# Kernel tuning notes

Measured on AMD Instinct MI355X. Metric: run time of the kernel, lower is better.

## Reference

```python
import jax, jax.numpy as jnp
import numpy as np

B, HH, WW = 8, 56, 56
N = HH * WW            # 3136 tokens
DIM, NH, SR = 512, 8, 7
HDIM = DIM // 2        # 256
LDIM = DIM - HDIM      # 256
DH = LDIM // NH        # 32
SCALE = DIM ** -0.5
EPS = 1e-5


def _dwconv(x, w):
    # depthwise 3x3, stride 1, SAME (= padding k//2): x [B,C,H,W], w [C,1,3,3]
    return jax.lax.conv_general_dilated(x, w, (1, 1), 'SAME',
                                        feature_group_count=x.shape[1],
                                        dimension_numbers=('NCHW', 'OIHW', 'NCHW'))


def _bn(x, g, b, m, v):
    # inference BatchNorm2d
    s = g * jax.lax.rsqrt(v + EPS)
    return (x - m[None, :, None, None]) * s[None, :, None, None] + b[None, :, None, None]


def _avg_pool(x, k):
    return jax.lax.reduce_window(x, 0.0, jax.lax.add, (1, 1, k, k), (1, 1, k, k), 'VALID') / (k * k)


def _max_pool(x, k):
    return jax.lax.reduce_window(x, -jnp.inf, jax.lax.max, (1, 1, k, k), (1, 1, k, k), 'VALID')


def setup_inputs() -> dict:
    key = jax.random.key(0)
    ks = jax.random.split(key, 32)
    d = {}
    d['x'] = jax.random.normal(ks[0], (B, N, DIM), jnp.float32)
    d['proj_v_w'] = jax.random.normal(ks[1], (LDIM, HDIM), jnp.float32) / np.sqrt(HDIM).astype(np.float32)
    d['conv1_w'] = jax.random.normal(ks[2], (LDIM, 1, 3, 3), jnp.float32) / 3.0
    d['conv2_w'] = jax.random.normal(ks[3], (LDIM, 1, 3, 3), jnp.float32) / 3.0
    d['conv3_w'] = jax.random.normal(ks[4], (HDIM, LDIM, 1, 1), jnp.float32) / np.sqrt(LDIM).astype(np.float32)
    d['conv3_b'] = jax.random.normal(ks[5], (HDIM,), jnp.float32) * 0.1
    d['v_conv_w'] = jax.random.normal(ks[6], (LDIM, 1, 3, 3), jnp.float32) / 3.0
    d['proj_w'] = jax.random.normal(ks[7], (DIM, DIM), jnp.float32) / np.sqrt(DIM).astype(np.float32)
    d['proj_b'] = jax.random.normal(ks[8], (DIM,), jnp.float32) * 0.1
    i = 9
    for pre, c in (('bn1', LDIM), ('bn2', LDIM), ('bn3', HDIM), ('vbn', LDIM)):
        d[pre + '_g'] = jax.random.uniform(ks[i], (c,), jnp.float32, 0.8, 1.2)
        d[pre + '_b'] = jax.random.normal(ks[i + 1], (c,), jnp.float32) * 0.1
        d[pre + '_m'] = jax.random.normal(ks[i + 2], (c,), jnp.float32) * 0.1
        d[pre + '_v'] = jax.random.uniform(ks[i + 3], (c,), jnp.float32, 0.5, 1.5)
        i += 4
    return d


def reference(x, proj_v_w, conv1_w, conv2_w, conv3_w, conv3_b, v_conv_w, proj_w, proj_b,
              bn1_g, bn1_b, bn1_m, bn1_v, bn2_g, bn2_b, bn2_m, bn2_v,
              bn3_g, bn3_b, bn3_m, bn3_v, vbn_g, vbn_b, vbn_m, vbn_v):
    x_high_in = x[..., :HDIM]                       # [B,N,HDIM]
    v = x_high_in @ proj_v_w.T                      # [B,N,LDIM]
    xh = v.reshape(B, HH, WW, LDIM).transpose(0, 3, 1, 2)   # [B,LDIM,H,W]
    xh = _bn(_dwconv(xh, conv1_w), bn1_g, bn1_b, bn1_m, bn1_v)
    q1 = _avg_pool(xh, SR)                          # [B,LDIM,8,8]
    q2 = _max_pool(xh, SR)
    xh = jax.nn.gelu(xh, approximate=False)
    xh = _bn(_dwconv(xh, conv2_w), bn2_g, bn2_b, bn2_m, bn2_v)
    k1 = _avg_pool(xh, SR)
    k2 = _max_pool(xh, SR)
    xh = jax.lax.conv_general_dilated(xh, conv3_w, (1, 1), 'SAME',
                                      dimension_numbers=('NCHW', 'OIHW', 'NCHW')) + conv3_b[None, :, None, None]
    xh = _bn(xh, bn3_g, bn3_b, bn3_m, bn3_v)
    xh = jax.nn.gelu(xh, approximate=False)
    x_high = xh.reshape(B, HDIM, N).transpose(0, 2, 1)      # [B,N,HDIM]

    hq, wq = HH // SR, WW // SR
    nq = hq * wq                                    # 64 pooled tokens

    def heads(t):                                   # [B,LDIM,hq,wq] -> [B,NH,nq,DH]
        return t.reshape(B, NH, DH, nq).transpose(0, 1, 3, 2)

    q = jnp.concatenate([heads(q1), heads(q2)], axis=-1)    # [B,NH,nq,2*DH]
    k = jnp.concatenate([heads(k1), heads(k2)], axis=-1)
    vh = v.reshape(B, N, NH, DH).transpose(0, 2, 1, 3)      # [B,NH,N,DH]

    attn = jnp.einsum('bhqd,bhkd->bhqk', q, k)              # [B,NH,nq,nq]
    attn = attn.reshape(B * NH, nq, hq, wq)
    attn = jax.image.resize(attn, (B * NH, nq, HH, WW), method='bilinear', antialias=False) * SCALE
    attn = attn.reshape(B, NH, nq, N)
    attn = jax.nn.softmax(attn, axis=-1)

    out = jnp.einsum('bhqn,bhnd->bhqd', attn, vh)           # [B,NH,nq,DH]
    out = out.reshape(B, NH, hq, wq, DH).transpose(0, 1, 4, 2, 3).reshape(B, LDIM, hq, wq)
    out = jax.image.resize(out, (B, LDIM, HH, WW), method='bilinear', antialias=False)
    out = _bn(_dwconv(out, v_conv_w), vbn_g, vbn_b, vbn_m, vbn_v)
    x_low = out.reshape(B, LDIM, N).transpose(0, 2, 1)      # [B,N,LDIM]

    y = jnp.concatenate([x_high, x_low], axis=-1) @ proj_w.T + proj_b
    return y
```

## Files before the change

### kernel.cpp

```cpp
#include <hip/hip_runtime.h>
#include <math.h>

#define BB 8
#define HH 56
#define WWD 56
#define NN 3136
#define CC 256
#define DIMM 512
#define NHEAD 8
#define NQ 64
#define EPSF 1e-5f
#define SCALEF 0.04419417382415922f

typedef __attribute__((ext_vector_type(8))) short short8;
typedef __attribute__((ext_vector_type(4))) short short4v;
typedef __attribute__((ext_vector_type(4))) float floatx4;

__device__ __forceinline__ float gelu_f(float x) {
    float z = x * 0.70710678118654752f;
    float a = fabsf(z);
    float t = __builtin_amdgcn_rcpf(1.f + 0.3275911f * a);
    float p = t * (0.254829592f + t * (-0.284496736f + t * (1.421413741f +
              t * (-1.453152027f + t * 1.061405429f))));
    float e = exp2f(-1.44269504f * a * a);
    float erfa = 1.f - p * e;
    float erfz = copysignf(erfa, z);
    return 0.5f * x * (1.f + erfz);
}
__device__ __forceinline__ unsigned short f2bf(float f) {
    union { float f; unsigned u; } v; v.f = f;
    return (unsigned short)((v.u + 0x7fffu + ((v.u >> 16) & 1u)) >> 16);
}
__device__ __forceinline__ float bf2f(unsigned short u) {
    union { unsigned u; float f; } v; v.u = ((unsigned)u) << 16;
    return v.f;
}

__global__ __launch_bounds__(256) void cast3_k(
    const float* __restrict__ a, const float* __restrict__ b,
    const float* __restrict__ cc, unsigned short* __restrict__ da,
    unsigned short* __restrict__ db, unsigned short* __restrict__ dc) {
    int i = blockIdx.x * 256 + threadIdx.x;
    if (i < 65536) {
        da[i] = f2bf(a[i]);
        db[i] = f2bf(b[i]);
    }
    if (i < 262144) dc[i] = f2bf(cc[i]);
}

__global__ __launch_bounds__(256) void gemm_v_mfma(
    const float* __restrict__ x, const unsigned short* __restrict__ w16,
    unsigned short* __restrict__ v16) {
    __shared__ short Ws[128 * 72];
    __shared__ short Xs[128 * 72];
    int n0 = blockIdx.x * 128, c0 = blockIdx.y * 128;
    int tid = threadIdx.x;
    int lane = tid & 63, wv = tid >> 6;
    int wc = wv >> 1, wn = wv & 1;
    int quad = lane >> 4, l16 = lane & 15;
    floatx4 zero = {0.f, 0.f, 0.f, 0.f};
    floatx4 acc[4][4];
#pragma unroll
    for (int ci = 0; ci < 4; ci++)
#pragma unroll
        for (int ni = 0; ni < 4; ni++) acc[ci][ni] = zero;

    for (int k0 = 0; k0 < 256; k0 += 64) {
        {
            int m = tid >> 1;
            int ob = (tid & 1) * 4;
            const float* src = x + (size_t)(n0 + m) * DIMM + k0 + ob * 8;
            short* dst = &Xs[m * 72 + ob * 8];
#pragma unroll
            for (int i2 = 0; i2 < 4; i2++) {
                floatx4 f0 = *(const floatx4*)(src + i2 * 8);
                floatx4 f1 = *(const floatx4*)(src + i2 * 8 + 4);
                short8 pk;
                pk[0] = (short)f2bf(f0[0]); pk[1] = (short)f2bf(f0[1]);
                pk[2] = (short)f2bf(f0[2]); pk[3] = (short)f2bf(f0[3]);
                pk[4] = (short)f2bf(f1[0]); pk[5] = (short)f2bf(f1[1]);
                pk[6] = (short)f2bf(f1[2]); pk[7] = (short)f2bf(f1[3]);
                *(short8*)(dst + i2 * 8) = pk;
            }
        }
#pragma unroll
        for (int i2 = 0; i2 < 4; i2++) {
            int idx = tid + 256 * i2;
            int c = idx >> 3, o = idx & 7;
            *(short8*)&Ws[c * 72 + o * 8] =
                *(const short8*)(const short*)(w16 + (size_t)(c0 + c) * 256 + k0 + o * 8);
        }
        __syncthreads();
#pragma unroll
        for (int kc = 0; kc < 2; kc++) {
            short8 af[4], bf[4];
#pragma unroll
            for (int ci = 0; ci < 4; ci++)
                af[ci] = *(const short8*)&Ws[(wc * 64 + ci * 16 + l16) * 72 + (kc * 4 + quad) * 8];
#pragma unroll
            for (int ni = 0; ni < 4; ni++)
                bf[ni] = *(const short8*)&Xs[(wn * 64 + ni * 16 + l16) * 72 + (kc * 4 + quad) * 8];
#pragma unroll
            for (int ci = 0; ci < 4; ci++)
#pragma unroll
                for (int ni = 0; ni < 4; ni++)
                    acc[ci][ni] = __builtin_amdgcn_mfma_f32_16x16x32_bf16(
                        af[ci], bf[ni], acc[ci][ni], 0, 0, 0);
        }
        __syncthreads();
    }
#pragma unroll
    for (int ni = 0; ni < 4; ni++) {
        int ng = n0 + wn * 64 + ni * 16 + l16;
        int b = ng / NN, n = ng - b * NN;
#pragma unroll
        for (int ci = 0; ci < 4; ci++) {
#pragma unroll
            for (int r = 0; r < 4; r++) {
                int c = c0 + wc * 64 + ci * 16 + quad * 4 + r;
                v16[((size_t)b * CC + c) * NN + n] = f2bf(acc[ci][ni][r]);
            }
        }
    }
}

__device__ __forceinline__ float dw3x3g(const float* __restrict__ Us, int lr,
                                        int x, bool ym, bool yp,
                                        float w0, float w1, float w2, float w3,
                                        float w4, float w5, float w6, float w7,
                                        float w8) {
    bool xm = x > 0, xp = x < 55;
    const float* r1 = &Us[(lr - 1) * 57 + x];
    const float* r2 = &Us[lr * 57 + x];
    const float* r3 = &Us[(lr + 1) * 57 + x];
    float acc = r2[0] * w4;
    if (xm) acc += r2[-1] * w3;
    if (xp) acc += r2[1] * w5;
    if (ym) {
        acc += r1[0] * w1;
        if (xm) acc += r1[-1] * w0;
        if (xp) acc += r1[1] * w2;
    }
    if (yp) {
        acc += r3[0] * w7;
        if (xm) acc += r3[-1] * w6;
        if (xp) acc += r3[1] * w8;
    }
    return acc;
}

__global__ __launch_bounds__(256) void dwconv2x_k(
    const unsigned short* __restrict__ in,
    const float* __restrict__ w1c, const float* __restrict__ g1,
    const float* __restrict__ b1, const float* __restrict__ m1,
    const float* __restrict__ v1,
    const float* __restrict__ w2c, const float* __restrict__ g2,
    const float* __restrict__ b2, const float* __restrict__ m2,
    const float* __restrict__ v2,
    unsigned short* __restrict__ out,
    float* __restrict__ oavg1, float* __restrict__ omax1,
    float* __restrict__ oavg2, float* __restrict__ omax2) {
    __shared__ float Us[18 * 57];
    __shared__ float Cs[16 * 57];
    int bid = blockIdx.x;
    int bc = bid >> 2, chunk = bid & 3;
    int c = bc & 255;
    int r0 = chunk * 14;
    int tid = threadIdx.x;
    const unsigned short* ip = in + (size_t)bc * NN;

    int gl0 = max(r0 - 2, 0), gh0 = min(r0 + 15, 55);
    int nin = (gh0 - gl0 + 1) * 56;
    const unsigned short* ipb = ip + gl0 * 56;
    {
        int e = tid * 4;
        if (e < nin) {
            short4v pk = *(const short4v*)(const short*)(ipb + e);
#pragma unroll
            for (int j = 0; j < 4; j++) {
                int el = e + j;
                int ry = el / 56, x = el - ry * 56;
                int lr = (gl0 + ry) - (r0 - 2);
                Us[lr * 57 + x] = bf2f((unsigned short)pk[j]);
            }
        }
    }
    float w0 = w1c[c * 9 + 0], w1 = w1c[c * 9 + 1], w2 = w1c[c * 9 + 2];
    float w3 = w1c[c * 9 + 3], w4 = w1c[c * 9 + 4], w5 = w1c[c * 9 + 5];
    float w6 = w1c[c * 9 + 6], w7 = w1c[c * 9 + 7], w8 = w1c[c * 9 + 8];
    float s = g1[c] * rsqrtf(v1[c] + EPSF);
    float sh = b1[c] - m1[c] * s;
    __syncthreads();
    int c1lo = max(r0 - 1, 0), c1hi = min(r0 + 14, 55);
    int n1 = (c1hi - c1lo + 1) * 56;
    for (int i = tid; i < n1; i += 256) {
        int ry = i / 56, x = i - ry * 56;
        int gr = c1lo + ry;
        int liu = gr - (r0 - 2);
        float acc = dw3x3g(Us, liu, x, gr > 0, gr < 55,
                           w0, w1, w2, w3, w4, w5, w6, w7, w8);
        Cs[(gr - (r0 - 1)) * 57 + x] = acc * s + sh;
    }
    __syncthreads();
    if (tid < 16) {
        int qy = 2 * chunk + (tid >> 3), qx = tid & 7;
        const float* p0 = &Cs[(qy * 7 - (r0 - 1)) * 57 + qx * 7];
        float sm = 0.f, mx = -INFINITY;
#pragma unroll
        for (int py = 0; py < 7; py++)
#pragma unroll
            for (int px = 0; px < 7; px++) {
                float t = p0[py * 57 + px];
                sm += t;
                mx = fmaxf(mx, t);
            }
        oavg1[(size_t)bc * 64 + qy * 8 + qx] = sm * (1.f / 49.f);
        omax1[(size_t)bc * 64 + qy * 8 + qx] = mx;
    }
    for (int i = tid; i < n1; i += 256) {
        int ry = i / 56, x = i - ry * 56;
        int lr1 = (c1lo + ry) - (r0 - 1);
        Us[lr1 * 57 + x] = gelu_f(Cs[lr1 * 57 + x]);
    }
    w0 = w2c[c * 9 + 0]; w1 = w2c[c * 9 + 1]; w2 = w2c[c * 9 + 2];
    w3 = w2c[c * 9 + 3]; w4 = w2c[c * 9 + 4]; w5 = w2c[c * 9 + 5];
    w6 = w2c[c * 9 + 6]; w7 = w2c[c * 9 + 7]; w8 = w2c[c * 9 + 8];
    s = g2[c] * rsqrtf(v2[c] + EPSF);
    sh = b2[c] - m2[c] * s;
    __syncthreads();
    unsigned short* op = out + (size_t)bc * NN;
    for (int i = tid; i < 14 * 56; i += 256) {
        int ry = i / 56, x = i - ry * 56;
        int gr = r0 + ry;
        int lg = ry + 1;
        float val = dw3x3g(Us, lg, x, gr > 0, gr < 55,
                           w0, w1, w2, w3, w4, w5, w6, w7, w8) * s + sh;
        Cs[ry * 57 + x] = val;
        op[gr * 56 + x] = f2bf(val);
    }
    __syncthreads();
    if (tid < 16) {
        int qy = 2 * chunk + (tid >> 3), qx = tid & 7;
        const float* p0 = &Cs[((qy * 7) - r0) * 57 + qx * 7];
        float sm = 0.f, mx = -INFINITY;
#pragma unroll
        for (int py = 0; py < 7; py++)
#pragma unroll
            for (int px = 0; px < 7; px++) {
                float t = p0[py * 57 + px];
                sm += t;
                mx = fmaxf(mx, t);
            }
        oavg2[(size_t)bc * 64 + qy * 8 + qx] = sm * (1.f / 49.f);
        omax2[(size_t)bc * 64 + qy * 8 + qx] = mx;
    }
}

__global__ __launch_bounds__(256) void conv3_mfma(
    const unsigned short* __restrict__ xin, const unsigned short* __restrict__ w16,
    const float* __restrict__ bias, const float* __restrict__ g,
    const float* __restrict__ bparm, const float* __restrict__ mm,
    const float* __restrict__ vvv, unsigned short* __restrict__ out16) {
    __shared__ short As[128 * 72];
    __shared__ short Bs[128 * 72];
    int m0 = blockIdx.x * 128, c0 = blockIdx.y * 128;
    int tid = threadIdx.x;
    int lane = tid & 63, wv = tid >> 6;
    int wm = wv >> 1, wc = wv & 1;
    int quad = lane >> 4, l16 = lane & 15;
    floatx4 zero = {0.f, 0.f, 0.f, 0.f};
    floatx4 acc[4][4];
#pragma unroll
    for (int mi = 0; mi < 4; mi++)
#pragma unroll
        for (int ci = 0; ci < 4; ci++) acc[mi][ci] = zero;

    for (int k0 = 0; k0 < 256; k0 += 64) {
        {
            int kk = lane >> 2, no = lane & 3;
            int rowb = wv * 32 + no * 8;
            int gn = m0 + rowb;
            int b8 = gn / NN, n8 = gn - b8 * NN;
#pragma unroll
            for (int ki = 0; ki < 4; ki++) {
                int c = k0 + ki * 16 + kk;
                short8 pk = *(const short8*)(const short*)(
                    xin + ((size_t)b8 * CC + c) * NN + n8);
                short* dst = &As[rowb * 72 + ki * 16 + kk];
#pragma unroll
                for (int j = 0; j < 8; j++) dst[j * 72] = pk[j];
            }
        }
#pragma unroll
        for (int i2 = 0; i2 < 4; i2++) {
            int idx = tid + 256 * i2;
            int c = idx >> 3, o = idx & 7;
            *(short8*)&Bs[c * 72 + o * 8] =
                *(const short8*)(const short*)(w16 + (size_t)(c0 + c) * CC + k0 + o * 8);
        }
        __syncthreads();
#pragma unroll
        for (int kc = 0; kc < 2; kc++) {
            short8 af[4], bf[4];
#pragma unroll
            for (int mi = 0; mi < 4; mi++)
                af[mi] = *(const short8*)&As[(wm * 64 + mi * 16 + l16) * 72 + (kc * 4 + quad) * 8];
#pragma unroll
            for (int ci = 0; ci < 4; ci++)
                bf[ci] = *(const short8*)&Bs[(wc * 64 + ci * 16 + l16) * 72 + (kc * 4 + quad) * 8];
#pragma unroll
            for (int mi = 0; mi < 4; mi++)
#pragma unroll
                for (int ci = 0; ci < 4; ci++)
                    acc[mi][ci] = __builtin_amdgcn_mfma_f32_16x16x32_bf16(
                        af[mi], bf[ci], acc[mi][ci], 0, 0, 0);
        }
        __syncthreads();
    }
#pragma unroll
    for (int ci = 0; ci < 4; ci++) {
        int co = c0 + wc * 64 + ci * 16 + l16;
        float s = g[co] * rsqrtf(vvv[co] + EPSF);
        float sh = bparm[co] - mm[co] * s;
        float bi = bias[co];
#pragma unroll
        for (int mi = 0; mi < 4; mi++) {
            int mbase = m0 + wm * 64 + mi * 16 + quad * 4;
#pragma unroll
            for (int r = 0; r < 4; r++) {
                float val = gelu_f((acc[mi][ci][r] + bi) * s + sh);
                out16[(size_t)(mbase + r) * CC + co] = f2bf(val);
            }
        }
    }
}

__global__ __launch_bounds__(256) void attn_qk_k(
    const float* __restrict__ q1, const float* __restrict__ q2,
    const float* __restrict__ k1, const float* __restrict__ k2,
    float* __restrict__ attn_s, float* __restrict__ mq) {
    int b = blockIdx.x >> 3, h = blockIdx.x & 7;
    __shared__ float Qs[64][64];
    __shared__ float Ks[64][64];
    __shared__ float pm[4][64];
    int tid = threadIdx.x;
#pragma unroll
    for (int l = 0; l < 16; l++) {
        int e = tid + 256 * l;
        int dt = e >> 6, i = e & 63;
        int d = dt & 31;
        const float* sq = (dt < 32) ? q1 : q2;
        const float* sk = (dt < 32) ? k1 : k2;
        Qs[dt][i] = sq[((size_t)b * CC + h * 32 + d) * NQ + i];
        Ks[dt][i] = sk[((size_t)b * CC + h * 32 + d) * NQ + i];
    }
    __syncthreads();
    int i = tid & 63, jg = tid >> 6;
    float acc[16] = {};
    for (int dt = 0; dt < 64; dt++) {
        float qv = Qs[dt][i];
#pragma unroll
        for (int t = 0; t < 16; t++) acc[t] += qv * Ks[dt][jg * 16 + t];
    }
    float mx = -INFINITY;
#pragma unroll
    for (int t = 0; t < 16; t++) {
        acc[t] *= SCALEF;
        mx = fmaxf(mx, acc[t]);
    }
    pm[jg][i] = mx;
    float* outp = attn_s + (((size_t)(b * 8 + h) * 64 + i) * 64) + jg * 16;
#pragma unroll
    for (int t = 0; t < 16; t++) outp[t] = acc[t];
    __syncthreads();
    if (tid < 64) {
        float m = fmaxf(fmaxf(pm[0][tid], pm[1][tid]),
                        fmaxf(pm[2][tid], pm[3][tid]));
        mq[(size_t)(b * 8 + h) * 64 + tid] = m;
    }
}

__global__ __launch_bounds__(256) void attn_pv_k(
    const float* __restrict__ attn_s, const float* __restrict__ mq,
    const unsigned short* __restrict__ v16,
    float* __restrict__ part_O, float* __restrict__ part_rs) {
    __shared__ float asub[64][68];
    __shared__ unsigned short Vs[32][456];
    __shared__ short po4[448][4];
    __shared__ float pw4[448][4];
    int s = blockIdx.x, bh = blockIdx.y;
    int b = bh >> 3, h = bh & 7;
    int tid = threadIdx.x;
    int lane = tid & 63, wv = tid >> 6;
    int quad = lane >> 4, l16 = lane & 15;
    int q = wv * 16 + l16;
    float Mv = mq[(size_t)bh * 64 + q];
    {
        int qq = tid & 63, jg = tid >> 6;
        const float* src = attn_s + ((size_t)bh * 64 + qq) * 64 + jg * 16;
        float* dst = &asub[qq][jg * 16];
#pragma unroll
        for (int t = 0; t < 4; t++)
            *(floatx4*)(dst + t * 4) = *(const floatx4*)(src + t * 4);
    }
    {
        int d = tid >> 3, o0 = tid & 7;
        const unsigned short* vp =
            v16 + ((size_t)(b * CC + h * 32 + d)) * NN + s * 448;
#pragma unroll
        for (int t = 0; t < 7; t++) {
            int oc = o0 + t * 8;
            *(short8*)&Vs[d][oc * 8] = *(const short8*)(const short*)(vp + oc * 8);
        }
    }
    for (int idx = tid; idx < 448; idx += 256) {
        int n = s * 448 + idx;
        int oy = n / WWD, ox = n - oy * WWD;
        float sy = (oy + 0.5f) * 0.14285714285714285f - 0.5f;
        float sx = (ox + 0.5f) * 0.14285714285714285f - 0.5f;
        float fy0 = floorf(sy), fx0 = floorf(sx);
        int y0 = (int)fy0, x0 = (int)fx0;
        float fy = sy - fy0, fx = sx - fx0;
        int y0c = max(y0, 0), y1c = min(y0 + 1, 7);
        int x0c = max(x0, 0), x1c = min(x0 + 1, 7);
        po4[idx][0] = (short)(y0c * 8 + x0c);
        po4[idx][1] = (short)(y0c * 8 + x1c);
        po4[idx][2] = (short)(y1c * 8 + x0c);
        po4[idx][3] = (short)(y1c * 8 + x1c);
        pw4[idx][0] = (1.f - fy) * (1.f - fx);
        pw4[idx][1] = (1.f - fy) * fx;
        pw4[idx][2] = fy * (1.f - fx);
        pw4[idx][3] = fy * fx;
    }
    __syncthreads();
    floatx4 zero = {0.f, 0.f, 0.f, 0.f};
    floatx4 acc0 = zero, acc1 = zero;
    float rsum = 0.f;
    for (int cch = 0; cch < 7; cch++) {
#pragma unroll
        for (int kc = 0; kc < 2; kc++) {
            int col = cch * 64 + kc * 32 + quad * 8;
            short8 af;
#pragma unroll
            for (int j = 0; j < 8; j++) {
                int np = col + j;
                float val = pw4[np][0] * asub[q][po4[np][0]]
                          + pw4[np][1] * asub[q][po4[np][1]]
                          + pw4[np][2] * asub[q][po4[np][2]]
                          + pw4[np][3] * asub[q][po4[np][3]];
                float p = exp2f((val - Mv) * 1.44269504f);
                rsum += p;
                af[j] = (short)f2bf(p);
            }
            short8 bf0 = *(const short8*)&Vs[l16][col];
            short8 bf1 = *(const short8*)&Vs[16 + l16][col];
            acc0 = __builtin_amdgcn_mfma_f32_16x16x32_bf16(af, bf0, acc0, 0, 0, 0);
            acc1 = __builtin_amdgcn_mfma_f32_16x16x32_bf16(af, bf1, acc1, 0, 0, 0);
        }
    }
    rsum += __shfl_xor(rsum, 16, 64);
    rsum += __shfl_xor(rsum, 32, 64);
    size_t base = ((size_t)bh * 7 + s) * 64;
    if (lane < 16) part_rs[base + wv * 16 + lane] = rsum;
#pragma unroll
    for (int nt = 0; nt < 2; nt++) {
        floatx4 a = nt ? acc1 : acc0;
#pragma unroll
        for (int r = 0; r < 4; r++) {
            int qo = wv * 16 + quad * 4 + r;
            part_O[(base + qo) * 32 + nt * 16 + l16] = a[r];
        }
    }
}

__global__ __launch_bounds__(256) void upconv_k(
    const float* __restrict__ part_O, const float* __restrict__ part_rs,
    const float* __restrict__ w,
    const float* __restrict__ g, const float* __restrict__ bparm,
    const float* __restrict__ m, const float* __restrict__ v,
    unsigned short* __restrict__ xlow16) {
    __shared__ float ts[64];
    __shared__ float Us[16 * 57];
    int bid = blockIdx.x;
    int bc = bid >> 2, chunk = bid & 3;
    int c = bc & 255;
    int r0 = chunk * 14;
    int tid = threadIdx.x;
    if (tid < 64) {
        int h = c >> 5, d = c & 31;
        int bh = (bc >> 8) * 8 + h;
        float o = 0.f, rs = 0.f;
        for (int s7 = 0; s7 < 7; s7++) {
            size_t base = ((size_t)bh * 7 + s7) * 64 + tid;
            o += part_O[base * 32 + d];
            rs += part_rs[base];
        }
        ts[tid] = o / rs;
    }
    __syncthreads();
    int blo = max(r0 - 1, 0), bhi = min(r0 + 14, 55);
    int nb = (bhi - blo + 1) * 56;
    for (int i = tid; i < nb; i += 256) {
        int ry = i / 56, x = i - ry * 56;
        int gr = blo + ry;
        float sy = (gr + 0.5f) * 0.14285714285714285f - 0.5f;
        float sx = (x + 0.5f) * 0.14285714285714285f - 0.5f;
        float fy0 = floorf(sy), fx0 = floorf(sx);
        int y0 = (int)fy0, x0 = (int)fx0;
        float fy = sy - fy0, fx = sx - fx0;
        int y0c = max(y0, 0), y1c = min(y0 + 1, 7);
        int x0c = max(x0, 0), x1c = min(x0 + 1, 7);
        float v00 = ts[y0c * 8 + x0c], v01 = ts[y0c * 8 + x1c];
        float v10 = ts[y1c * 8 + x0c], v11 = ts[y1c * 8 + x1c];
        Us[(gr - (r0 - 1)) * 57 + x] =
            (1.f - fy) * ((1.f - fx) * v00 + fx * v01) +
            fy * ((1.f - fx) * v10 + fx * v11);
    }
    float w0 = w[c * 9 + 0], w1 = w[c * 9 + 1], w2 = w[c * 9 + 2];
    float w3 = w[c * 9 + 3], w4 = w[c * 9 + 4], w5 = w[c * 9 + 5];
    float w6 = w[c * 9 + 6], w7 = w[c * 9 + 7], w8 = w[c * 9 + 8];
    float s = g[c] * rsqrtf(v[c] + EPSF);
    float sh = bparm[c] - m[c] * s;
    __syncthreads();
    unsigned short* op = xlow16 + (size_t)bc * NN;
    for (int i = tid; i < 14 * 56; i += 256) {
        int ry = i / 56, x = i - ry * 56;
        int gr = r0 + ry;
        float val = dw3x3g(Us, ry + 1, x, gr > 0, gr < 55,
                           w0, w1, w2, w3, w4, w5, w6, w7, w8);
        op[gr * 56 + x] = f2bf(val * s + sh);
    }
}

__global__ __launch_bounds__(256) void proj_mfma(
    const unsigned short* __restrict__ xh16, const unsigned short* __restrict__ xl16,
    const unsigned short* __restrict__ w16, const float* __restrict__ bias,
    float* __restrict__ y) {
    __shared__ short As[128 * 72];
    __shared__ short Bs[128 * 72];
    int m0 = blockIdx.x * 128, c0 = blockIdx.y * 128;
    int tid = threadIdx.x;
    int lane = tid & 63, wv = tid >> 6;
    int wm = wv >> 1, wc = wv & 1;
    int quad = lane >> 4, l16 = lane & 15;
    floatx4 zero = {0.f, 0.f, 0.f, 0.f};
    floatx4 acc[4][4];
#pragma unroll
    for (int mi = 0; mi < 4; mi++)
#pragma unroll
        for (int ci = 0; ci < 4; ci++) acc[mi][ci] = zero;

    for (int k0 = 0; k0 < 512; k0 += 64) {
        if (k0 < 256) {
#pragma unroll
            for (int i2 = 0; i2 < 4; i2++) {
                int idx = tid + 256 * i2;
                int m = idx >> 3, o = idx & 7;
                *(short8*)&As[m * 72 + o * 8] =
                    *(const short8*)(const short*)(xh16 + (size_t)(m0 + m) * CC + k0 + o * 8);
            }
        } else {
            int kk = lane >> 2, no = lane & 3;
            int rowb = wv * 32 + no * 8;
            int gn = m0 + rowb;
            int b8 = gn / NN, n8 = gn - b8 * NN;
#pragma unroll
            for (int ki = 0; ki < 4; ki++) {
                int c = (k0 - 256) + ki * 16 + kk;
                short8 pk = *(const short8*)(const short*)(
                    xl16 + ((size_t)b8 * CC + c) * NN + n8);
                short* dst = &As[rowb * 72 + ki * 16 + kk];
#pragma unroll
                for (int j = 0; j < 8; j++) dst[j * 72] = pk[j];
            }
        }
#pragma unroll
        for (int i2 = 0; i2 < 4; i2++) {
            int idx = tid + 256 * i2;
            int c = idx >> 3, o = idx & 7;
            *(short8*)&Bs[c * 72 + o * 8] =
                *(const short8*)(const short*)(w16 + (size_t)(c0 + c) * DIMM + k0 + o * 8);
        }
        __syncthreads();
#pragma unroll
        for (int kc = 0; kc < 2; kc++) {
            short8 af[4], bf[4];
#pragma unroll
            for (int mi = 0; mi < 4; mi++)
                af[mi] = *(const short8*)&As[(wm * 64 + mi * 16 + l16) * 72 + (kc * 4 + quad) * 8];
#pragma unroll
            for (int ci = 0; ci < 4; ci++)
                bf[ci] = *(const short8*)&Bs[(wc * 64 + ci * 16 + l16) * 72 + (kc * 4 + quad) * 8];
#pragma unroll
            for (int mi = 0; mi < 4; mi++)
#pragma unroll
                for (int ci = 0; ci < 4; ci++)
                    acc[mi][ci] = __builtin_amdgcn_mfma_f32_16x16x32_bf16(
                        af[mi], bf[ci], acc[mi][ci], 0, 0, 0);
        }
        __syncthreads();
    }
#pragma unroll
    for (int mi = 0; mi < 4; mi++) {
        int mbase = m0 + wm * 64 + mi * 16 + quad * 4;
#pragma unroll
        for (int ci = 0; ci < 4; ci++) {
            int co = c0 + wc * 64 + ci * 16 + l16;
            float bi = bias[co];
#pragma unroll
            for (int r = 0; r < 4; r++)
                y[(size_t)(mbase + r) * DIMM + co] = acc[mi][ci][r] + bi;
        }
    }
}

extern "C" void kernel_launch(void* const* d_in, const int* in_sizes, int n_in,
                              void* d_out, int out_size, void* d_ws, size_t ws_size,
                              hipStream_t stream) {
    const float* x        = (const float*)d_in[0];
    const float* proj_v_w = (const float*)d_in[1];
    const float* conv1_w  = (const float*)d_in[2];
    const float* conv2_w  = (const float*)d_in[3];
    const float* conv3_w  = (const float*)d_in[4];
    const float* conv3_b  = (const float*)d_in[5];
    const float* v_conv_w = (const float*)d_in[6];
    const float* proj_w   = (const float*)d_in[7];
    const float* proj_b   = (const float*)d_in[8];
    const float* bn1_g = (const float*)d_in[9],  *bn1_b = (const float*)d_in[10];
    const float* bn1_m = (const float*)d_in[11], *bn1_v = (const float*)d_in[12];
    const float* bn2_g = (const float*)d_in[13], *bn2_b = (const float*)d_in[14];
    const float* bn2_m = (const float*)d_in[15], *bn2_v = (const float*)d_in[16];
    const float* bn3_g = (const float*)d_in[17], *bn3_b = (const float*)d_in[18];
    const float* bn3_m = (const float*)d_in[19], *bn3_v = (const float*)d_in[20];
    const float* vbn_g = (const float*)d_in[21], *vbn_b = (const float*)d_in[22];
    const float* vbn_m = (const float*)d_in[23], *vbn_v = (const float*)d_in[24];

    const size_t big = (size_t)BB * CC * NN;
    unsigned short* v16    = (unsigned short*)d_ws;
    unsigned short* bufA16 = v16 + big;
    unsigned short* bufB16 = bufA16 + big;
    unsigned short* xh16   = bufB16 + big;
    unsigned short* xlow16 = xh16 + big;
    float* small = (float*)(xlow16 + big);
    float* q1 = small;
    float* q2 = q1 + (size_t)BB * CC * NQ;
    float* k1 = q2 + (size_t)BB * CC * NQ;
    float* k2 = k1 + (size_t)BB * CC * NQ;
    float* attn_s = k2 + (size_t)BB * CC * NQ;
    float* out_s  = attn_s + (size_t)BB * NHEAD * NQ * NQ;
    float* part_O = out_s + (size_t)BB * CC * NQ;
    float* part_rs = part_O + (size_t)64 * 7 * 64 * 32;
    float* mq = part_rs + (size_t)64 * 7 * 64;
    unsigned short* w16v  = (unsigned short*)(mq + 64 * 64);
    unsigned short* w16c3 = w16v + 65536;
    unsigned short* w16p  = w16c3 + 65536;

    cast3_k<<<1024, 256, 0, stream>>>(proj_v_w, conv3_w, proj_w, w16v, w16c3, w16p);

    gemm_v_mfma<<<dim3(196, 2), 256, 0, stream>>>(x, w16v, v16);
    dwconv2x_k<<<BB * CC * 4, 256, 0, stream>>>(
        v16, conv1_w, bn1_g, bn1_b, bn1_m, bn1_v,
        conv2_w, bn2_g, bn2_b, bn2_m, bn2_v, bufB16, q1, q2, k1, k2);
    conv3_mfma<<<dim3(196, 2), 256, 0, stream>>>(bufB16, w16c3, conv3_b,
                                                 bn3_g, bn3_b, bn3_m, bn3_v, xh16);
    attn_qk_k<<<64, 256, 0, stream>>>(q1, q2, k1, k2, attn_s, mq);
    attn_pv_k<<<dim3(7, 64), 256, 0, stream>>>(attn_s, mq, v16, part_O, part_rs);
    upconv_k<<<BB * CC * 4, 256, 0, stream>>>(part_O, part_rs, v_conv_w,
                                              vbn_g, vbn_b, vbn_m, vbn_v, xlow16);
    proj_mfma<<<dim3(196, 4), 256, 0, stream>>>(xh16, xlow16, w16p, proj_b,
                                                (float*)d_out);
}
```

Baseline: 265.3 us.

## Fuse conv3 GEMM with attention QK and PV into one heterogeneous launch

```diff
diff --git a/kernel.cpp b/kernel.cpp
--- a/kernel.cpp
+++ b/kernel.cpp
@@ -256,14 +256,15 @@
     }
 }
 
-__global__ __launch_bounds__(256) void conv3_mfma(
+__device__ void conv3_body(
+    char* smem, int mct,
     const unsigned short* __restrict__ xin, const unsigned short* __restrict__ w16,
     const float* __restrict__ bias, const float* __restrict__ g,
     const float* __restrict__ bparm, const float* __restrict__ mm,
     const float* __restrict__ vvv, unsigned short* __restrict__ out16) {
-    __shared__ short As[128 * 72];
-    __shared__ short Bs[128 * 72];
-    int m0 = blockIdx.x * 128, c0 = blockIdx.y * 128;
+    short* As = (short*)smem;
+    short* Bs = (short*)(smem + 18432);
+    int m0 = (mct % 196) * 128, c0 = (mct / 196) * 128;
     int tid = threadIdx.x;
     int lane = tid & 63, wv = tid >> 6;
     int wm = wv >> 1, wc = wv & 1;
@@ -335,15 +336,27 @@
     }
 }
 
-__global__ __launch_bounds__(256) void attn_qk_k(
+__global__ __launch_bounds__(256) void conv3_pvqk_k(
+    const unsigned short* __restrict__ xin, const unsigned short* __restrict__ w16,
+    const float* __restrict__ bias, const float* __restrict__ g,
+    const float* __restrict__ bparm, const float* __restrict__ mm,
+    const float* __restrict__ vvv, unsigned short* __restrict__ out16,
     const float* __restrict__ q1, const float* __restrict__ q2,
     const float* __restrict__ k1, const float* __restrict__ k2,
-    float* __restrict__ attn_s, float* __restrict__ mq) {
-    int b = blockIdx.x >> 3, h = blockIdx.x & 7;
-    __shared__ float Qs[64][64];
-    __shared__ float Ks[64][64];
-    __shared__ float pm[4][64];
+    const unsigned short* __restrict__ v16,
+    float* __restrict__ part_O, float* __restrict__ part_rs) {
+    __shared__ __align__(16) char smem[57344];
+    int bid = blockIdx.x;
     int tid = threadIdx.x;
+    if (bid < 392) {
+        conv3_body(smem, bid, xin, w16, bias, g, bparm, mm, vvv, out16);
+        return;
+    }
+    int pid = bid - 392;
+    int s = pid % 7, bh = pid / 7;
+    int b = bh >> 3, h = bh & 7;
+    float (*Qs)[64] = (float(*)[64])smem;
+    float (*Ks)[64] = (float(*)[64])(smem + 16384);
 #pragma unroll
     for (int l = 0; l < 16; l++) {
         int e = tid + 256 * l;
@@ -356,7 +369,9 @@
     }
     __syncthreads();
     int i = tid & 63, jg = tid >> 6;
-    float acc[16] = {};
+    float acc[16];
+#pragma unroll
+    for (int t = 0; t < 16; t++) acc[t] = 0.f;
     for (int dt = 0; dt < 64; dt++) {
         float qv = Qs[dt][i];
 #pragma unroll
@@ -368,41 +383,21 @@
         acc[t] *= SCALEF;
         mx = fmaxf(mx, acc[t]);
     }
-    pm[jg][i] = mx;
-    float* outp = attn_s + (((size_t)(b * 8 + h) * 64 + i) * 64) + jg * 16;
-#pragma unroll
-    for (int t = 0; t < 16; t++) outp[t] = acc[t];
-    __syncthreads();
-    if (tid < 64) {
-        float m = fmaxf(fmaxf(pm[0][tid], pm[1][tid]),
-                        fmaxf(pm[2][tid], pm[3][tid]));
-        mq[(size_t)(b * 8 + h) * 64 + tid] = m;
-    }
-}
-
-__global__ __launch_bounds__(256) void attn_pv_k(
-    const float* __restrict__ attn_s, const float* __restrict__ mq,
-    const unsigned short* __restrict__ v16,
-    float* __restrict__ part_O, float* __restrict__ part_rs) {
-    __shared__ float asub[64][68];
-    __shared__ unsigned short Vs[32][456];
-    __shared__ short po4[448][4];
-    __shared__ float pw4[448][4];
-    int s = blockIdx.x, bh = blockIdx.y;
-    int b = bh >> 3, h = bh & 7;
-    int tid = threadIdx.x;
+    __syncthreads();
+    float (*asub)[68] = (float(*)[68])smem;
+    unsigned short (*Vs)[456] = (unsigned short(*)[456])(smem + 17408);
+    short (*po4)[4] = (short(*)[4])(smem + 46592);
+    float (*pw4)[4] = (float(*)[4])(smem + 50176);
+    float* pm = (float*)(smem + 46592);
+#pragma unroll
+    for (int t = 0; t < 16; t++) asub[i][jg * 16 + t] = acc[t];
+    pm[jg * 64 + i] = mx;
+    __syncthreads();
     int lane = tid & 63, wv = tid >> 6;
     int quad = lane >> 4, l16 = lane & 15;
     int q = wv * 16 + l16;
-    float Mv = mq[(size_t)bh * 64 + q];
-    {
-        int qq = tid & 63, jg = tid >> 6;
-        const float* src = attn_s + ((size_t)bh * 64 + qq) * 64 + jg * 16;
-        float* dst = &asub[qq][jg * 16];
-#pragma unroll
-        for (int t = 0; t < 4; t++)
-            *(floatx4*)(dst + t * 4) = *(const floatx4*)(src + t * 4);
-    }
+    float Mv = fmaxf(fmaxf(pm[q], pm[64 + q]), fmaxf(pm[128 + q], pm[192 + q]));
+    __syncthreads();
     {
         int d = tid >> 3, o0 = tid & 7;
         const unsigned short* vp =
@@ -661,10 +656,9 @@
     dwconv2x_k<<<BB * CC * 4, 256, 0, stream>>>(
         v16, conv1_w, bn1_g, bn1_b, bn1_m, bn1_v,
         conv2_w, bn2_g, bn2_b, bn2_m, bn2_v, bufB16, q1, q2, k1, k2);
-    conv3_mfma<<<dim3(196, 2), 256, 0, stream>>>(bufB16, w16c3, conv3_b,
-                                                 bn3_g, bn3_b, bn3_m, bn3_v, xh16);
-    attn_qk_k<<<64, 256, 0, stream>>>(q1, q2, k1, k2, attn_s, mq);
-    attn_pv_k<<<dim3(7, 64), 256, 0, stream>>>(attn_s, mq, v16, part_O, part_rs);
+    conv3_pvqk_k<<<392 + 448, 256, 0, stream>>>(
+        bufB16, w16c3, conv3_b, bn3_g, bn3_b, bn3_m, bn3_v, xh16,
+        q1, q2, k1, k2, v16, part_O, part_rs);
     upconv_k<<<BB * CC * 4, 256, 0, stream>>>(part_O, part_rs, v_conv_w,
                                               vbn_g, vbn_b, vbn_m, vbn_v, xlow16);
     proj_mfma<<<dim3(196, 4), 256, 0, stream>>>(xh16, xlow16, w16p, proj_b,
```

Result: slower. 277.9 us (+4.7%).
